# Kernel tuning notes

Measured on AMD Instinct MI355X. Metric: run time of the kernel, lower is better.

Reference implementation:

```python
import jax, jax.numpy as jnp
import numpy as np

N_NODES = 100000
N_EDGES = 1600000
D_IN = 128
D_OUT = 128


def setup_inputs() -> dict:
    key = jax.random.key(0)
    k1, k2, k3, k4, k5 = jax.random.split(key, 5)
    x = jax.random.normal(k1, (N_NODES, D_IN), dtype=jnp.float32)
    edge_row = jax.random.randint(k2, (N_EDGES,), 0, N_NODES, dtype=jnp.int32)
    edge_col = jax.random.randint(k3, (N_EDGES,), 0, N_NODES, dtype=jnp.int32)
    edge_vals = jax.random.uniform(k4, (N_EDGES,), dtype=jnp.float32)
    stdv = 1.0 / np.sqrt(D_OUT)
    weight = jax.random.uniform(k5, (D_IN, D_OUT), dtype=jnp.float32,
                                minval=-stdv, maxval=stdv)
    return {"x": x, "edge_row": edge_row, "edge_col": edge_col,
            "edge_vals": edge_vals, "weight": weight}


def reference(x, edge_row, edge_col, edge_vals, weight):
    # spmm(adj, x): gather source features, scale by edge weight, segment-sum to dst
    n = x.shape[0]
    msgs = x[edge_col] * edge_vals[:, None]          # [E, D_IN]
    agg = jax.ops.segment_sum(msgs, edge_row, num_segments=n)  # [N, D_IN]
    # dense weight matmul
    return agg @ weight                               # [N, D_OUT]
```

## Files before the change

kernel.cpp:

```cpp
#include <hip/hip_runtime.h>
#include <hip/hip_fp16.h>


#define N_NODES 100000
#define N_EDGES 1600000
#define DIM     128
#define BROWS   32
#define CB      3125
#define CAP     1024
#define EPB     4096
#define PBLK    392

#define OFF_CCNT   25600000
#define OFF_CSTART 25612800
#define OFF_CCUR   25625600
#define OFF_EBUF1  25638400

__global__ __launch_bounds__(256) void gemm_xw_kernel(
    const float* __restrict__ x,
    const float* __restrict__ W,
    __half*      __restrict__ y)
{
    __shared__ float As[32 * 32];
    __shared__ float Ws[32 * 128];

    const int t    = threadIdx.x;
    const int row0 = blockIdx.x * 32;
    const int r0   = (t >> 5) * 4;
    const int c0   = (t & 31) * 4;

    float acc[4][4];
#pragma unroll
    for (int i = 0; i < 4; ++i)
#pragma unroll
        for (int j = 0; j < 4; ++j) acc[i][j] = 0.f;

    for (int k0 = 0; k0 < 128; k0 += 32) {
        {
            int r  = t >> 3;
            int kp = t & 7;
            float4 a = *(const float4*)(x + (size_t)(row0 + r) * 128 + k0 + kp * 4);
            *(float4*)(As + r * 32 + kp * 4) = a;
        }
        {
            const float4* Wg = (const float4*)(W + (size_t)k0 * 128);
            float4* Wl = (float4*)Ws;
#pragma unroll
            for (int i = 0; i < 4; ++i) Wl[t + 256 * i] = Wg[t + 256 * i];
        }
        __syncthreads();

#pragma unroll
        for (int kk = 0; kk < 32; ++kk) {
            float4 w = *(const float4*)(Ws + kk * 128 + c0);
            float a0 = As[(r0 + 0) * 32 + kk];
            float a1 = As[(r0 + 1) * 32 + kk];
            float a2 = As[(r0 + 2) * 32 + kk];
            float a3 = As[(r0 + 3) * 32 + kk];
            acc[0][0] += a0 * w.x; acc[0][1] += a0 * w.y; acc[0][2] += a0 * w.z; acc[0][3] += a0 * w.w;
            acc[1][0] += a1 * w.x; acc[1][1] += a1 * w.y; acc[1][2] += a1 * w.z; acc[1][3] += a1 * w.w;
            acc[2][0] += a2 * w.x; acc[2][1] += a2 * w.y; acc[2][2] += a2 * w.z; acc[2][3] += a2 * w.w;
            acc[3][0] += a3 * w.x; acc[3][1] += a3 * w.y; acc[3][2] += a3 * w.z; acc[3][3] += a3 * w.w;
        }
        __syncthreads();
    }

#pragma unroll
    for (int i = 0; i < 4; ++i) {
        __half2 p0 = __floats2half2_rn(acc[i][0], acc[i][1]);
        __half2 p1 = __floats2half2_rn(acc[i][2], acc[i][3]);
        uint2 w;
        w.x = *(const unsigned*)&p0;
        w.y = *(const unsigned*)&p1;
        *(uint2*)(y + (size_t)(row0 + r0 + i) * 128 + c0) = w;
    }
}

__global__ __launch_bounds__(256) void zero_ccnt_kernel(unsigned* ccnt) {
    int i = blockIdx.x * 256 + threadIdx.x;
    if (i < CB) ccnt[i] = 0u;
}

__global__ __launch_bounds__(256) void coarse_hist_kernel(
    const int* __restrict__ erow, unsigned* __restrict__ ccnt)
{
    __shared__ unsigned lh[CB];
    const int t = threadIdx.x;
    const unsigned e0 = blockIdx.x * (unsigned)EPB;
    for (int i = t; i < CB; i += 256) lh[i] = 0u;
    __syncthreads();
#pragma unroll 4
    for (int k = 0; k < EPB / 256; ++k) {
        unsigned e = e0 + k * 256u + t;
        if (e < N_EDGES) atomicAdd(&lh[(unsigned)erow[e] >> 5], 1u);
    }
    __syncthreads();
    for (int i = t; i < CB; i += 256) {
        unsigned h = lh[i];
        if (h) atomicAdd(&ccnt[i], h);
    }
}

__global__ __launch_bounds__(1024) void coarse_scan_kernel(
    const unsigned* __restrict__ ccnt,
    unsigned* __restrict__ cstart,
    unsigned* __restrict__ ccur)
{
    __shared__ unsigned wsum[16];
    const int t  = threadIdx.x;
    const int i0 = 4 * t;
    unsigned v0 = (i0 + 0 < CB) ? ccnt[i0 + 0] : 0u;
    unsigned v1 = (i0 + 1 < CB) ? ccnt[i0 + 1] : 0u;
    unsigned v2 = (i0 + 2 < CB) ? ccnt[i0 + 2] : 0u;
    unsigned v3 = (i0 + 3 < CB) ? ccnt[i0 + 3] : 0u;
    unsigned s  = v0 + v1 + v2 + v3;
    unsigned inc = s;
#pragma unroll
    for (int d = 1; d < 64; d <<= 1) {
        unsigned o = __shfl_up(inc, d);
        if ((t & 63) >= d) inc += o;
    }
    if ((t & 63) == 63) wsum[t >> 6] = inc;
    __syncthreads();
    if (t == 0) {
        unsigned run = 0;
#pragma unroll
        for (int w = 0; w < 16; ++w) { unsigned sw = wsum[w]; wsum[w] = run; run += sw; }
        cstart[CB] = run;
    }
    __syncthreads();
    unsigned excl = inc - s + wsum[t >> 6];
    if (i0 + 0 < CB) { cstart[i0 + 0] = excl;                ccur[i0 + 0] = excl;                }
    if (i0 + 1 < CB) { cstart[i0 + 1] = excl + v0;           ccur[i0 + 1] = excl + v0;           }
    if (i0 + 2 < CB) { cstart[i0 + 2] = excl + v0 + v1;      ccur[i0 + 2] = excl + v0 + v1;      }
    if (i0 + 3 < CB) { cstart[i0 + 3] = excl + v0 + v1 + v2; ccur[i0 + 3] = excl + v0 + v1 + v2; }
}

__global__ __launch_bounds__(256) void partition_kernel(
    const int*   __restrict__ erow,
    const int*   __restrict__ ecol,
    const float* __restrict__ eval,
    unsigned*    __restrict__ ccur,
    uint2*       __restrict__ ebuf1)
{
    __shared__ unsigned hist[CB];
    __shared__ unsigned gbase[CB];
    const int t = threadIdx.x;
    const unsigned e0 = blockIdx.x * (unsigned)EPB;

    for (int i = t; i < CB; i += 256) hist[i] = 0u;
    __syncthreads();

#pragma unroll 4
    for (int k = 0; k < EPB / 256; ++k) {
        unsigned e = e0 + k * 256u + t;
        if (e < N_EDGES) atomicAdd(&hist[(unsigned)erow[e] >> 5], 1u);
    }
    __syncthreads();

    for (int i = t; i < CB; i += 256) {
        unsigned h = hist[i];
        gbase[i] = h ? atomicAdd(&ccur[i], h) : 0u;
        hist[i] = 0u;
    }
    __syncthreads();

#pragma unroll 4
    for (int k = 0; k < EPB / 256; ++k) {
        unsigned e = e0 + k * 256u + t;
        if (e < N_EDGES) {
            unsigned r = (unsigned)erow[e];
            unsigned b = r >> 5;
            unsigned rank = atomicAdd(&hist[b], 1u);
            ebuf1[gbase[b] + rank] =
                make_uint2(((r & 31u) << 17) | (unsigned)ecol[e],
                           __float_as_uint(eval[e]));
        }
    }
}

__global__ __launch_bounds__(256) void bucket_agg_kernel(
    const __half*   __restrict__ y,
    const unsigned* __restrict__ cstart,
    const uint2*    __restrict__ ebuf1,
    float*          __restrict__ out)
{
    __shared__ uint2    raw[CAP];
    __shared__ uint2    sorted[CAP];
    __shared__ unsigned hist[BROWS];
    __shared__ unsigned sstart[BROWS];
    __shared__ unsigned scur[BROWS];

    const int t    = threadIdx.x;
    const int b    = blockIdx.x;
    const int lane = t & 63;
    const int wv   = t >> 6;
    const unsigned lo = cstart[b];
    const unsigned hi = cstart[b + 1];
    const unsigned n  = (hi > lo) ? (hi - lo) : 0u;
    const unsigned nchunks = n ? (n + CAP - 1) / CAP : 1u;

    for (unsigned c = 0; c < nchunks; ++c) {
        const unsigned base = lo + c * CAP;
        const unsigned m = (n > c * CAP) ? (((n - c * CAP) < CAP) ? (n - c * CAP) : CAP) : 0u;

        if (t < BROWS) hist[t] = 0u;
        __syncthreads();

        for (unsigned i = t; i < m; i += 256) {
            uint2 rec = ebuf1[base + i];
            raw[i] = rec;
            atomicAdd(&hist[rec.x >> 17], 1u);
        }
        __syncthreads();

        if (t < 64) {
            unsigned v = (t < BROWS) ? hist[t] : 0u;
            unsigned inc = v;
#pragma unroll
            for (int d = 1; d < 64; d <<= 1) {
                unsigned o = __shfl_up(inc, d);
                if (t >= d) inc += o;
            }
            unsigned excl = inc - v;
            if (t < BROWS) { sstart[t] = excl; scur[t] = excl; }
        }
        __syncthreads();

        for (unsigned i = t; i < m; i += 256) {
            uint2 rec = raw[i];
            unsigned p = atomicAdd(&scur[rec.x >> 17], 1u);
            sorted[p] = rec;
        }
        __syncthreads();

        for (int r = wv; r < BROWS; r += 4) {
            int row = b * BROWS + r;
            if (row >= N_NODES) break;
            float ax, ay;
            if (c == 0) { ax = 0.f; ay = 0.f; }
            else {
                float2 p = *((const float2*)(out + (size_t)row * 128) + lane);
                ax = p.x; ay = p.y;
            }
            unsigned j = sstart[r], e = scur[r];
            for (; j + 4 <= e; j += 4) {
                uint2 r0 = sorted[j + 0];
                uint2 r1 = sorted[j + 1];
                uint2 r2 = sorted[j + 2];
                uint2 r3 = sorted[j + 3];
                const __half2 h0 = *((const __half2*)(y + (size_t)(r0.x & 0x1FFFFu) * 128) + lane);
                const __half2 h1 = *((const __half2*)(y + (size_t)(r1.x & 0x1FFFFu) * 128) + lane);
                const __half2 h2 = *((const __half2*)(y + (size_t)(r2.x & 0x1FFFFu) * 128) + lane);
                const __half2 h3 = *((const __half2*)(y + (size_t)(r3.x & 0x1FFFFu) * 128) + lane);
                float v0 = __uint_as_float(r0.y);
                float v1 = __uint_as_float(r1.y);
                float v2 = __uint_as_float(r2.y);
                float v3 = __uint_as_float(r3.y);
                float2 f0 = __half22float2(h0);
                float2 f1 = __half22float2(h1);
                float2 f2 = __half22float2(h2);
                float2 f3 = __half22float2(h3);
                ax = fmaf(f0.x, v0, ax); ay = fmaf(f0.y, v0, ay);
                ax = fmaf(f1.x, v1, ax); ay = fmaf(f1.y, v1, ay);
                ax = fmaf(f2.x, v2, ax); ay = fmaf(f2.y, v2, ay);
                ax = fmaf(f3.x, v3, ax); ay = fmaf(f3.y, v3, ay);
            }
            for (; j < e; ++j) {
                uint2 rr = sorted[j];
                const __half2 h = *((const __half2*)(y + (size_t)(rr.x & 0x1FFFFu) * 128) + lane);
                float v = __uint_as_float(rr.y);
                float2 f = __half22float2(h);
                ax = fmaf(f.x, v, ax); ay = fmaf(f.y, v, ay);
            }
            *((float2*)(out + (size_t)row * 128) + lane) = make_float2(ax, ay);
        }
        __syncthreads();
    }
}

extern "C" void kernel_launch(void* const* d_in, const int* in_sizes, int n_in,
                              void* d_out, int out_size, void* d_ws, size_t ws_size,
                              hipStream_t stream) {
    const float* x    = (const float*)d_in[0];
    const int*   erow = (const int*)d_in[1];
    const int*   ecol = (const int*)d_in[2];
    const float* eval = (const float*)d_in[3];
    const float* W    = (const float*)d_in[4];
    float* out = (float*)d_out;

    char* ws = (char*)d_ws;
    __half*   y      = (__half*)  (ws);
    unsigned* ccnt   = (unsigned*)(ws + OFF_CCNT);
    unsigned* cstart = (unsigned*)(ws + OFF_CSTART);
    unsigned* ccur   = (unsigned*)(ws + OFF_CCUR);
    uint2*    ebuf1  = (uint2*)   (ws + OFF_EBUF1);

    gemm_xw_kernel<<<N_NODES / 32, 256, 0, stream>>>(x, W, y);
    zero_ccnt_kernel<<<(CB + 255) / 256, 256, 0, stream>>>(ccnt);
    coarse_hist_kernel<<<PBLK, 256, 0, stream>>>(erow, ccnt);
    coarse_scan_kernel<<<1, 1024, 0, stream>>>(ccnt, cstart, ccur);
    partition_kernel<<<PBLK, 256, 0, stream>>>(erow, ecol, eval, ccur, ebuf1);
    bucket_agg_kernel<<<CB, 256, 0, stream>>>(y, cstart, ebuf1, out);
}
```

Measured before the change: 293.2 us.

## Fuse coarse histogram into GEMM and simplify partition to global atomics

The coarse row-bucket histogram is folded into the X·W GEMM kernel: each of its 3125 blocks counts 512 edges with direct global atomics, so the separate histogram launch goes away. The partition kernel drops its shared-memory histogram and two-pass block-local ranking. Each thread now loads 4 edges and claims output slots with one global atomicAdd per edge. This cuts launches, shared-memory passes and extra reads of erow, but adds heavy global atomic contention on 3125 counters and makes the order of edges within a bucket nondeterministic.

```diff
diff --git a/kernel.cpp b/kernel.cpp
--- a/kernel.cpp
+++ b/kernel.cpp
@@ -8,26 +8,31 @@
 #define BROWS   32
 #define CB      3125
 #define CAP     1024
-#define EPB     4096
-#define PBLK    392
 
 #define OFF_CCNT   25600000
 #define OFF_CSTART 25612800
 #define OFF_CCUR   25625600
 #define OFF_EBUF1  25638400
 
-__global__ __launch_bounds__(256) void gemm_xw_kernel(
+__global__ __launch_bounds__(256) void gemm_xw_hist_kernel(
     const float* __restrict__ x,
     const float* __restrict__ W,
-    __half*      __restrict__ y)
+    const int*   __restrict__ erow,
+    __half*      __restrict__ y,
+    unsigned*    __restrict__ ccnt)
 {
     __shared__ float As[32 * 32];
     __shared__ float Ws[32 * 128];
 
     const int t    = threadIdx.x;
     const int row0 = blockIdx.x * 32;
-    const int r0   = (t >> 5) * 4;
-    const int c0   = (t & 31) * 4;
+
+    const unsigned e0  = (unsigned)blockIdx.x * 512u + (unsigned)t;
+    const unsigned re0 = (unsigned)erow[e0];
+    const unsigned re1 = (unsigned)erow[e0 + 256u];
+
+    const int r0 = (t >> 5) * 4;
+    const int c0 = (t & 31) * 4;
 
     float acc[4][4];
 #pragma unroll
@@ -65,6 +70,9 @@
         __syncthreads();
     }
 
+    atomicAdd(&ccnt[re0 >> 5], 1u);
+    atomicAdd(&ccnt[re1 >> 5], 1u);
+
 #pragma unroll
     for (int i = 0; i < 4; ++i) {
         __half2 p0 = __floats2half2_rn(acc[i][0], acc[i][1]);
@@ -79,26 +87,6 @@
 __global__ __launch_bounds__(256) void zero_ccnt_kernel(unsigned* ccnt) {
     int i = blockIdx.x * 256 + threadIdx.x;
     if (i < CB) ccnt[i] = 0u;
-}
-
-__global__ __launch_bounds__(256) void coarse_hist_kernel(
-    const int* __restrict__ erow, unsigned* __restrict__ ccnt)
-{
-    __shared__ unsigned lh[CB];
-    const int t = threadIdx.x;
-    const unsigned e0 = blockIdx.x * (unsigned)EPB;
-    for (int i = t; i < CB; i += 256) lh[i] = 0u;
-    __syncthreads();
-#pragma unroll 4
-    for (int k = 0; k < EPB / 256; ++k) {
-        unsigned e = e0 + k * 256u + t;
-        if (e < N_EDGES) atomicAdd(&lh[(unsigned)erow[e] >> 5], 1u);
-    }
-    __syncthreads();
-    for (int i = t; i < CB; i += 256) {
-        unsigned h = lh[i];
-        if (h) atomicAdd(&ccnt[i], h);
-    }
 }
 
 __global__ __launch_bounds__(1024) void coarse_scan_kernel(
@@ -136,6 +124,8 @@
     if (i0 + 3 < CB) { cstart[i0 + 3] = excl + v0 + v1 + v2; ccur[i0 + 3] = excl + v0 + v1 + v2; }
 }
 
+#define PEPT 4
+#define PBLK ((N_EDGES + 256 * PEPT - 1) / (256 * PEPT))
 __global__ __launch_bounds__(256) void partition_kernel(
     const int*   __restrict__ erow,
     const int*   __restrict__ ecol,
@@ -143,40 +133,29 @@
     unsigned*    __restrict__ ccur,
     uint2*       __restrict__ ebuf1)
 {
-    __shared__ unsigned hist[CB];
-    __shared__ unsigned gbase[CB];
-    const int t = threadIdx.x;
-    const unsigned e0 = blockIdx.x * (unsigned)EPB;
-
-    for (int i = t; i < CB; i += 256) hist[i] = 0u;
-    __syncthreads();
-
-#pragma unroll 4
-    for (int k = 0; k < EPB / 256; ++k) {
-        unsigned e = e0 + k * 256u + t;
-        if (e < N_EDGES) atomicAdd(&hist[(unsigned)erow[e] >> 5], 1u);
-    }
-    __syncthreads();
-
-    for (int i = t; i < CB; i += 256) {
-        unsigned h = hist[i];
-        gbase[i] = h ? atomicAdd(&ccur[i], h) : 0u;
-        hist[i] = 0u;
-    }
-    __syncthreads();
-
-#pragma unroll 4
-    for (int k = 0; k < EPB / 256; ++k) {
-        unsigned e = e0 + k * 256u + t;
-        if (e < N_EDGES) {
-            unsigned r = (unsigned)erow[e];
-            unsigned b = r >> 5;
-            unsigned rank = atomicAdd(&hist[b], 1u);
-            ebuf1[gbase[b] + rank] =
-                make_uint2(((r & 31u) << 17) | (unsigned)ecol[e],
-                           __float_as_uint(eval[e]));
-        }
-    }
+    const unsigned base = blockIdx.x * (256u * PEPT) + threadIdx.x;
+
+    unsigned r[PEPT], c[PEPT], vb[PEPT];
+    bool     ok[PEPT];
+#pragma unroll
+    for (int k = 0; k < PEPT; ++k) {
+        unsigned e = base + 256u * k;
+        ok[k] = (e < N_EDGES);
+        unsigned es = ok[k] ? e : (N_EDGES - 1);
+        r[k]  = (unsigned)erow[es];
+        c[k]  = (unsigned)ecol[es];
+        vb[k] = __float_as_uint(eval[es]);
+    }
+
+    unsigned p[PEPT];
+#pragma unroll
+    for (int k = 0; k < PEPT; ++k)
+        if (ok[k]) p[k] = atomicAdd(&ccur[r[k] >> 5], 1u);
+
+#pragma unroll
+    for (int k = 0; k < PEPT; ++k)
+        if (ok[k])
+            ebuf1[p[k]] = make_uint2(((r[k] & 31u) << 17) | c[k], vb[k]);
 }
 
 __global__ __launch_bounds__(256) void bucket_agg_kernel(
@@ -296,9 +275,8 @@
     unsigned* ccur   = (unsigned*)(ws + OFF_CCUR);
     uint2*    ebuf1  = (uint2*)   (ws + OFF_EBUF1);
 
-    gemm_xw_kernel<<<N_NODES / 32, 256, 0, stream>>>(x, W, y);
     zero_ccnt_kernel<<<(CB + 255) / 256, 256, 0, stream>>>(ccnt);
-    coarse_hist_kernel<<<PBLK, 256, 0, stream>>>(erow, ccnt);
+    gemm_xw_hist_kernel<<<N_NODES / 32, 256, 0, stream>>>(x, W, erow, y, ccnt);
     coarse_scan_kernel<<<1, 1024, 0, stream>>>(ccnt, cstart, ccur);
     partition_kernel<<<PBLK, 256, 0, stream>>>(erow, ecol, eval, ccur, ebuf1);
     bucket_agg_kernel<<<CB, 256, 0, stream>>>(y, cstart, ebuf1, out);
```

Measured after the change: 453.5 us. 54.6% more time.

## Split edge partition into two passes over 160-row superbuckets

Applied to the files above, without the earlier changes.

The single 3125-bucket partition is replaced by a coarse partition into 625 superbuckets of 160 rows, followed by a per-superbucket in-place shared-memory scatter into five 32-row buckets. The coarse histogram now uses direct global atomics on padded counters instead of shared-memory block histograms. The aim is smaller per-block shared histograms and more coalesced scatter writes in the partition step. In exchange it adds an extra kernel pass over the edge buffer, and partition2 silently caps each superbucket at 3072 edges, which is a correctness risk if a superbucket overflows.

```diff
diff --git a/kernel.cpp b/kernel.cpp
--- a/kernel.cpp
+++ b/kernel.cpp
@@ -8,13 +8,16 @@
 #define BROWS   32
 #define CB      3125
 #define CAP     1024
-#define EPB     4096
-#define PBLK    392
+#define NSB     625
+#define SBROWS  160
+#define FPS     5
+#define CAP2    3072
+#define CPAD    16
 
 #define OFF_CCNT   25600000
-#define OFF_CSTART 25612800
-#define OFF_CCUR   25625600
-#define OFF_EBUF1  25638400
+#define OFF_CSTART 25800000
+#define OFF_CSB    25812544
+#define OFF_EBUF1  25852544
 
 __global__ __launch_bounds__(256) void gemm_xw_kernel(
     const float* __restrict__ x,
@@ -78,41 +81,35 @@
 
 __global__ __launch_bounds__(256) void zero_ccnt_kernel(unsigned* ccnt) {
     int i = blockIdx.x * 256 + threadIdx.x;
-    if (i < CB) ccnt[i] = 0u;
-}
-
-__global__ __launch_bounds__(256) void coarse_hist_kernel(
+    if (i < CB) ccnt[i * CPAD] = 0u;
+}
+
+#define HEPT 4
+#define HBLK ((N_EDGES + 256 * HEPT - 1) / (256 * HEPT))
+__global__ __launch_bounds__(256) void hist_kernel(
     const int* __restrict__ erow, unsigned* __restrict__ ccnt)
 {
-    __shared__ unsigned lh[CB];
-    const int t = threadIdx.x;
-    const unsigned e0 = blockIdx.x * (unsigned)EPB;
-    for (int i = t; i < CB; i += 256) lh[i] = 0u;
-    __syncthreads();
-#pragma unroll 4
-    for (int k = 0; k < EPB / 256; ++k) {
-        unsigned e = e0 + k * 256u + t;
-        if (e < N_EDGES) atomicAdd(&lh[(unsigned)erow[e] >> 5], 1u);
-    }
-    __syncthreads();
-    for (int i = t; i < CB; i += 256) {
-        unsigned h = lh[i];
-        if (h) atomicAdd(&ccnt[i], h);
+    const unsigned base = blockIdx.x * (256u * HEPT) + threadIdx.x;
+#pragma unroll
+    for (int k = 0; k < HEPT; ++k) {
+        unsigned e = base + 256u * k;
+        if (e < N_EDGES)
+            atomicAdd(&ccnt[((unsigned)erow[e] >> 5) * CPAD], 1u);
     }
 }
 
 __global__ __launch_bounds__(1024) void coarse_scan_kernel(
     const unsigned* __restrict__ ccnt,
     unsigned* __restrict__ cstart,
-    unsigned* __restrict__ ccur)
+    unsigned* __restrict__ ccur_sb)
 {
     __shared__ unsigned wsum[16];
     const int t  = threadIdx.x;
     const int i0 = 4 * t;
-    unsigned v0 = (i0 + 0 < CB) ? ccnt[i0 + 0] : 0u;
-    unsigned v1 = (i0 + 1 < CB) ? ccnt[i0 + 1] : 0u;
-    unsigned v2 = (i0 + 2 < CB) ? ccnt[i0 + 2] : 0u;
-    unsigned v3 = (i0 + 3 < CB) ? ccnt[i0 + 3] : 0u;
+    unsigned v0 = (i0 + 0 < CB) ? ccnt[(i0 + 0) * CPAD] : 0u;
+    unsigned v1 = (i0 + 1 < CB) ? ccnt[(i0 + 1) * CPAD] : 0u;
+    unsigned v2 = (i0 + 2 < CB) ? ccnt[(i0 + 2) * CPAD] : 0u;
+    unsigned v3 = (i0 + 3 < CB) ? ccnt[(i0 + 3) * CPAD] : 0u;
     unsigned s  = v0 + v1 + v2 + v3;
     unsigned inc = s;
 #pragma unroll
@@ -130,52 +127,85 @@
     }
     __syncthreads();
     unsigned excl = inc - s + wsum[t >> 6];
-    if (i0 + 0 < CB) { cstart[i0 + 0] = excl;                ccur[i0 + 0] = excl;                }
-    if (i0 + 1 < CB) { cstart[i0 + 1] = excl + v0;           ccur[i0 + 1] = excl + v0;           }
-    if (i0 + 2 < CB) { cstart[i0 + 2] = excl + v0 + v1;      ccur[i0 + 2] = excl + v0 + v1;      }
-    if (i0 + 3 < CB) { cstart[i0 + 3] = excl + v0 + v1 + v2; ccur[i0 + 3] = excl + v0 + v1 + v2; }
-}
-
-__global__ __launch_bounds__(256) void partition_kernel(
+    unsigned ex[4] = { excl, excl + v0, excl + v0 + v1, excl + v0 + v1 + v2 };
+#pragma unroll
+    for (int j = 0; j < 4; ++j) {
+        int idx = i0 + j;
+        if (idx < CB) {
+            cstart[idx] = ex[j];
+            if (idx % FPS == 0) ccur_sb[(idx / FPS) * CPAD] = ex[j];
+        }
+    }
+}
+
+#define EPB1  4096
+#define PBLK1 ((N_EDGES + EPB1 - 1) / EPB1)
+__global__ __launch_bounds__(256) void partition1_kernel(
     const int*   __restrict__ erow,
     const int*   __restrict__ ecol,
     const float* __restrict__ eval,
-    unsigned*    __restrict__ ccur,
+    unsigned*    __restrict__ ccur_sb,
     uint2*       __restrict__ ebuf1)
 {
-    __shared__ unsigned hist[CB];
-    __shared__ unsigned gbase[CB];
+    __shared__ unsigned hist[NSB];
+    __shared__ unsigned gbase[NSB];
     const int t = threadIdx.x;
-    const unsigned e0 = blockIdx.x * (unsigned)EPB;
-
-    for (int i = t; i < CB; i += 256) hist[i] = 0u;
+    const unsigned e0 = blockIdx.x * (unsigned)EPB1;
+
+    for (int i = t; i < NSB; i += 256) hist[i] = 0u;
     __syncthreads();
 
 #pragma unroll 4
-    for (int k = 0; k < EPB / 256; ++k) {
+    for (int k = 0; k < EPB1 / 256; ++k) {
         unsigned e = e0 + k * 256u + t;
-        if (e < N_EDGES) atomicAdd(&hist[(unsigned)erow[e] >> 5], 1u);
-    }
-    __syncthreads();
-
-    for (int i = t; i < CB; i += 256) {
+        if (e < N_EDGES) atomicAdd(&hist[(unsigned)erow[e] / SBROWS], 1u);
+    }
+    __syncthreads();
+
+    for (int i = t; i < NSB; i += 256) {
         unsigned h = hist[i];
-        gbase[i] = h ? atomicAdd(&ccur[i], h) : 0u;
+        gbase[i] = h ? atomicAdd(&ccur_sb[i * CPAD], h) : 0u;
         hist[i] = 0u;
     }
     __syncthreads();
 
 #pragma unroll 4
-    for (int k = 0; k < EPB / 256; ++k) {
+    for (int k = 0; k < EPB1 / 256; ++k) {
         unsigned e = e0 + k * 256u + t;
         if (e < N_EDGES) {
             unsigned r = (unsigned)erow[e];
-            unsigned b = r >> 5;
-            unsigned rank = atomicAdd(&hist[b], 1u);
-            ebuf1[gbase[b] + rank] =
-                make_uint2(((r & 31u) << 17) | (unsigned)ecol[e],
+            unsigned s = r / SBROWS;
+            unsigned rank = atomicAdd(&hist[s], 1u);
+            ebuf1[gbase[s] + rank] =
+                make_uint2(((r - s * SBROWS) << 17) | (unsigned)ecol[e],
                            __float_as_uint(eval[e]));
         }
+    }
+}
+
+__global__ __launch_bounds__(256) void partition2_kernel(
+    const unsigned* __restrict__ cstart,
+    uint2*          __restrict__ ebuf1)
+{
+    __shared__ uint2    raw[CAP2];
+    __shared__ unsigned scur[FPS];
+
+    const int t  = threadIdx.x;
+    const int sb = blockIdx.x;
+    const unsigned base = cstart[sb * FPS];
+    unsigned n2 = cstart[sb * FPS + FPS] - base;
+    if (n2 > CAP2) n2 = CAP2;
+
+    if (t < FPS) scur[t] = cstart[sb * FPS + t] - base;
+
+    for (unsigned i = t; i < n2; i += 256) raw[i] = ebuf1[base + i];
+    __syncthreads();
+
+    for (unsigned i = t; i < n2; i += 256) {
+        uint2 rec = raw[i];
+        unsigned f = rec.x >> 22;
+        unsigned d = atomicAdd(&scur[f], 1u);
+        ebuf1[base + d] = rec;
     }
 }
 
@@ -210,7 +240,7 @@
         for (unsigned i = t; i < m; i += 256) {
             uint2 rec = ebuf1[base + i];
             raw[i] = rec;
-            atomicAdd(&hist[rec.x >> 17], 1u);
+            atomicAdd(&hist[(rec.x >> 17) & 31u], 1u);
         }
         __syncthreads();
 
@@ -229,7 +259,7 @@
 
         for (unsigned i = t; i < m; i += 256) {
             uint2 rec = raw[i];
-            unsigned p = atomicAdd(&scur[rec.x >> 17], 1u);
+            unsigned p = atomicAdd(&scur[(rec.x >> 17) & 31u], 1u);
             sorted[p] = rec;
         }
         __syncthreads();
@@ -290,16 +320,17 @@
     float* out = (float*)d_out;
 
     char* ws = (char*)d_ws;
-    __half*   y      = (__half*)  (ws);
-    unsigned* ccnt   = (unsigned*)(ws + OFF_CCNT);
-    unsigned* cstart = (unsigned*)(ws + OFF_CSTART);
-    unsigned* ccur   = (unsigned*)(ws + OFF_CCUR);
-    uint2*    ebuf1  = (uint2*)   (ws + OFF_EBUF1);
+    __half*   y       = (__half*)  (ws);
+    unsigned* ccnt    = (unsigned*)(ws + OFF_CCNT);
+    unsigned* cstart  = (unsigned*)(ws + OFF_CSTART);
+    unsigned* ccur_sb = (unsigned*)(ws + OFF_CSB);
+    uint2*    ebuf1   = (uint2*)   (ws + OFF_EBUF1);
 
     gemm_xw_kernel<<<N_NODES / 32, 256, 0, stream>>>(x, W, y);
     zero_ccnt_kernel<<<(CB + 255) / 256, 256, 0, stream>>>(ccnt);
-    coarse_hist_kernel<<<PBLK, 256, 0, stream>>>(erow, ccnt);
-    coarse_scan_kernel<<<1, 1024, 0, stream>>>(ccnt, cstart, ccur);
-    partition_kernel<<<PBLK, 256, 0, stream>>>(erow, ecol, eval, ccur, ebuf1);
+    hist_kernel<<<HBLK, 256, 0, stream>>>(erow, ccnt);
+    coarse_scan_kernel<<<1, 1024, 0, stream>>>(ccnt, cstart, ccur_sb);
+    partition1_kernel<<<PBLK1, 256, 0, stream>>>(erow, ecol, eval, ccur_sb, ebuf1);
+    partition2_kernel<<<NSB, 256, 0, stream>>>(cstart, ebuf1);
     bucket_agg_kernel<<<CB, 256, 0, stream>>>(y, cstart, ebuf1, out);
 }
```

After: 348.9 us. 1.19x slower.

## Replace global-atomic coarse histogram with per-block partials plus reduction, pad cursors

Applied to the files above, without the earlier changes.

The coarse histogram now has each block write its full per-bucket partial histogram to workspace, and a separate reduce kernel sums the partials column-wise. This replaces the zeroing kernel and the global atomics. The per-bucket cursors are padded to 16-word stride to avoid atomic contention on the same cache lines. Loads in the histogram and partition kernels are batched ahead of the LDS atomics to expose memory-level parallelism. The cost is an extra kernel launch, a reduction that reads roughly 625x3125 words, and reuse of the ebuf1 region as scratch for the partials.

```diff
diff --git a/kernel.cpp b/kernel.cpp
--- a/kernel.cpp
+++ b/kernel.cpp
@@ -8,13 +8,19 @@
 #define BROWS   32
 #define CB      3125
 #define CAP     1024
-#define EPB     4096
-#define PBLK    392
+#define CPAD    16
+
+#define HBLKS    625
+#define HPB      2560
+#define HSTRIDE  3200
+
+#define EPB  4096
+#define PBLK ((N_EDGES + EPB - 1) / EPB)
 
 #define OFF_CCNT   25600000
 #define OFF_CSTART 25612800
 #define OFF_CCUR   25625600
-#define OFF_EBUF1  25638400
+#define OFF_EBUF1  25825600
 
 __global__ __launch_bounds__(256) void gemm_xw_kernel(
     const float* __restrict__ x,
@@ -76,29 +82,39 @@
     }
 }
 
-__global__ __launch_bounds__(256) void zero_ccnt_kernel(unsigned* ccnt) {
-    int i = blockIdx.x * 256 + threadIdx.x;
-    if (i < CB) ccnt[i] = 0u;
-}
-
-__global__ __launch_bounds__(256) void coarse_hist_kernel(
-    const int* __restrict__ erow, unsigned* __restrict__ ccnt)
+__global__ __launch_bounds__(256) void histp_kernel(
+    const int* __restrict__ erow, unsigned* __restrict__ hpart)
 {
     __shared__ unsigned lh[CB];
     const int t = threadIdx.x;
-    const unsigned e0 = blockIdx.x * (unsigned)EPB;
+    const unsigned e0 = blockIdx.x * (unsigned)HPB;
+
     for (int i = t; i < CB; i += 256) lh[i] = 0u;
     __syncthreads();
-#pragma unroll 4
-    for (int k = 0; k < EPB / 256; ++k) {
-        unsigned e = e0 + k * 256u + t;
-        if (e < N_EDGES) atomicAdd(&lh[(unsigned)erow[e] >> 5], 1u);
-    }
-    __syncthreads();
-    for (int i = t; i < CB; i += 256) {
-        unsigned h = lh[i];
-        if (h) atomicAdd(&ccnt[i], h);
-    }
+
+    unsigned b[10];
+#pragma unroll
+    for (int k = 0; k < 10; ++k)
+        b[k] = (unsigned)erow[e0 + k * 256u + t] >> 5;
+#pragma unroll
+    for (int k = 0; k < 10; ++k)
+        atomicAdd(&lh[b[k]], 1u);
+    __syncthreads();
+
+    unsigned* row = hpart + (size_t)blockIdx.x * HSTRIDE;
+    for (int i = t; i < CB; i += 256) row[i] = lh[i];
+}
+
+__global__ __launch_bounds__(256) void reduce_kernel(
+    const unsigned* __restrict__ hpart, unsigned* __restrict__ ccnt)
+{
+    int j = blockIdx.x * 256 + threadIdx.x;
+    if (j >= CB) return;
+    const unsigned* p = hpart + j;
+    unsigned s = 0;
+#pragma unroll 5
+    for (int b = 0; b < HBLKS; ++b) s += p[(size_t)b * HSTRIDE];
+    ccnt[j] = s;
 }
 
 __global__ __launch_bounds__(1024) void coarse_scan_kernel(
@@ -130,10 +146,15 @@
     }
     __syncthreads();
     unsigned excl = inc - s + wsum[t >> 6];
-    if (i0 + 0 < CB) { cstart[i0 + 0] = excl;                ccur[i0 + 0] = excl;                }
-    if (i0 + 1 < CB) { cstart[i0 + 1] = excl + v0;           ccur[i0 + 1] = excl + v0;           }
-    if (i0 + 2 < CB) { cstart[i0 + 2] = excl + v0 + v1;      ccur[i0 + 2] = excl + v0 + v1;      }
-    if (i0 + 3 < CB) { cstart[i0 + 3] = excl + v0 + v1 + v2; ccur[i0 + 3] = excl + v0 + v1 + v2; }
+    unsigned ex[4] = { excl, excl + v0, excl + v0 + v1, excl + v0 + v1 + v2 };
+#pragma unroll
+    for (int j = 0; j < 4; ++j) {
+        int idx = i0 + j;
+        if (idx < CB) {
+            cstart[idx] = ex[j];
+            ccur[idx * CPAD] = ex[j];
+        }
+    }
 }
 
 __global__ __launch_bounds__(256) void partition_kernel(
@@ -151,30 +172,46 @@
     for (int i = t; i < CB; i += 256) hist[i] = 0u;
     __syncthreads();
 
-#pragma unroll 4
-    for (int k = 0; k < EPB / 256; ++k) {
-        unsigned e = e0 + k * 256u + t;
-        if (e < N_EDGES) atomicAdd(&hist[(unsigned)erow[e] >> 5], 1u);
+    for (int kb = 0; kb < 4; ++kb) {
+        unsigned rr[4]; bool ok[4];
+#pragma unroll
+        for (int u = 0; u < 4; ++u) {
+            unsigned e = e0 + (unsigned)(kb * 4 + u) * 256u + t;
+            ok[u] = (e < N_EDGES);
+            rr[u] = ok[u] ? (unsigned)erow[e] : 0u;
+        }
+#pragma unroll
+        for (int u = 0; u < 4; ++u)
+            if (ok[u]) atomicAdd(&hist[rr[u] >> 5], 1u);
     }
     __syncthreads();
 
     for (int i = t; i < CB; i += 256) {
         unsigned h = hist[i];
-        gbase[i] = h ? atomicAdd(&ccur[i], h) : 0u;
+        gbase[i] = h ? atomicAdd(&ccur[i * CPAD], h) : 0u;
         hist[i] = 0u;
     }
     __syncthreads();
 
-#pragma unroll 4
-    for (int k = 0; k < EPB / 256; ++k) {
-        unsigned e = e0 + k * 256u + t;
-        if (e < N_EDGES) {
-            unsigned r = (unsigned)erow[e];
-            unsigned b = r >> 5;
-            unsigned rank = atomicAdd(&hist[b], 1u);
-            ebuf1[gbase[b] + rank] =
-                make_uint2(((r & 31u) << 17) | (unsigned)ecol[e],
-                           __float_as_uint(eval[e]));
+    for (int kb = 0; kb < 4; ++kb) {
+        unsigned rr[4], cc[4], vv[4]; bool ok[4];
+#pragma unroll
+        for (int u = 0; u < 4; ++u) {
+            unsigned e = e0 + (unsigned)(kb * 4 + u) * 256u + t;
+            ok[u] = (e < N_EDGES);
+            unsigned es = ok[u] ? e : (N_EDGES - 1);
+            rr[u] = (unsigned)erow[es];
+            cc[u] = (unsigned)ecol[es];
+            vv[u] = __float_as_uint(eval[es]);
+        }
+#pragma unroll
+        for (int u = 0; u < 4; ++u) {
+            if (ok[u]) {
+                unsigned bkt  = rr[u] >> 5;
+                unsigned rank = atomicAdd(&hist[bkt], 1u);
+                ebuf1[gbase[bkt] + rank] =
+                    make_uint2(((rr[u] & 31u) << 17) | cc[u], vv[u]);
+            }
         }
     }
 }
@@ -210,7 +247,7 @@
         for (unsigned i = t; i < m; i += 256) {
             uint2 rec = ebuf1[base + i];
             raw[i] = rec;
-            atomicAdd(&hist[rec.x >> 17], 1u);
+            atomicAdd(&hist[(rec.x >> 17) & 31u], 1u);
         }
         __syncthreads();
 
@@ -229,7 +266,7 @@
 
         for (unsigned i = t; i < m; i += 256) {
             uint2 rec = raw[i];
-            unsigned p = atomicAdd(&scur[rec.x >> 17], 1u);
+            unsigned p = atomicAdd(&scur[(rec.x >> 17) & 31u], 1u);
             sorted[p] = rec;
         }
         __syncthreads();
@@ -295,10 +332,11 @@
     unsigned* cstart = (unsigned*)(ws + OFF_CSTART);
     unsigned* ccur   = (unsigned*)(ws + OFF_CCUR);
     uint2*    ebuf1  = (uint2*)   (ws + OFF_EBUF1);
+    unsigned* hpart  = (unsigned*)(ws + OFF_EBUF1);
 
     gemm_xw_kernel<<<N_NODES / 32, 256, 0, stream>>>(x, W, y);
-    zero_ccnt_kernel<<<(CB + 255) / 256, 256, 0, stream>>>(ccnt);
-    coarse_hist_kernel<<<PBLK, 256, 0, stream>>>(erow, ccnt);
+    histp_kernel<<<HBLKS, 256, 0, stream>>>(erow, hpart);
+    reduce_kernel<<<(CB + 255) / 256, 256, 0, stream>>>(hpart, ccnt);
     coarse_scan_kernel<<<1, 1024, 0, stream>>>(ccnt, cstart, ccur);
     partition_kernel<<<PBLK, 256, 0, stream>>>(erow, ecol, eval, ccur, ebuf1);
     bucket_agg_kernel<<<CB, 256, 0, stream>>>(y, cstart, ebuf1, out);
```

New measurement: 340.2 us. 1.16x slower.
